# Performance work log

Hardware: AMD Instinct MI355X
Metric: run time of the kernel (lower is better)

Reference implementation:

```python
import jax, jax.numpy as jnp
import numpy as np

N = 100000
E = 1600000
F_IN = 128
HID = 16
HEADS = 8
NCLS = 2
NGRAPH = 64
NEG_SLOPE = 0.2


def setup_inputs() -> dict:
    key = jax.random.key(0)
    ks = jax.random.split(key, 12)
    x = jax.random.normal(ks[0], (N, F_IN), dtype=jnp.float32)
    edge_index = jax.random.randint(ks[1], (2, E), 0, N, dtype=jnp.int64)
    batch = jnp.sort(jax.random.randint(ks[2], (N,), 0, NGRAPH, dtype=jnp.int64))
    s1 = 1.0 / np.sqrt(F_IN)
    s2 = 1.0 / np.sqrt(HEADS * HID)
    W1 = jax.random.normal(ks[3], (F_IN, HEADS * HID), dtype=jnp.float32) * s1
    att_src1 = jax.random.normal(ks[4], (HEADS, HID), dtype=jnp.float32) * s2
    att_dst1 = jax.random.normal(ks[5], (HEADS, HID), dtype=jnp.float32) * s2
    b1 = jnp.zeros((HEADS * HID,), dtype=jnp.float32)
    W2 = jax.random.normal(ks[6], (HEADS * HID, 1 * NCLS), dtype=jnp.float32) * s2
    att_src2 = jax.random.normal(ks[7], (1, NCLS), dtype=jnp.float32)
    att_dst2 = jax.random.normal(ks[8], (1, NCLS), dtype=jnp.float32)
    b2 = jnp.zeros((NCLS,), dtype=jnp.float32)
    return {"x": x, "edge_index": edge_index, "batch": batch,
            "W1": W1, "att_src1": att_src1, "att_dst1": att_dst1, "b1": b1,
            "W2": W2, "att_src2": att_src2, "att_dst2": att_dst2, "b2": b2}


def _gat_conv(x, src, dst, W, att_src, att_dst, bias, heads, out_dim, concat):
    # x: [N, Fin]; src/dst: [E'] (self-loops already appended)
    h = (x @ W).reshape(N, heads, out_dim)              # [N, H, D]
    a_src = jnp.sum(h * att_src[None], axis=-1)          # [N, H]
    a_dst = jnp.sum(h * att_dst[None], axis=-1)          # [N, H]
    e = a_src[src] + a_dst[dst]                          # [E', H]
    e = jnp.where(e >= 0, e, NEG_SLOPE * e)              # leaky_relu
    # softmax over incoming edges of each destination node
    emax = jax.ops.segment_max(e, dst, num_segments=N)   # [N, H]
    ee = jnp.exp(e - emax[dst])
    denom = jax.ops.segment_sum(ee, dst, num_segments=N)
    alpha = ee / denom[dst]                              # [E', H]
    msg = h[src] * alpha[:, :, None]                     # [E', H, D]
    out = jax.ops.segment_sum(msg, dst, num_segments=N)  # [N, H, D]
    if concat:
        out = out.reshape(N, heads * out_dim)
    else:
        out = out.mean(axis=1)
    return out + bias


def reference(x, edge_index, batch, W1, att_src1, att_dst1, b1, W2, att_src2, att_dst2, b2):
    # add self-loops (PyG GATConv default add_self_loops=True)
    loop = jnp.arange(N, dtype=edge_index.dtype)
    src = jnp.concatenate([edge_index[0], loop])
    dst = jnp.concatenate([edge_index[1], loop])

    h = _gat_conv(x, src, dst, W1, att_src1, att_dst1, b1, HEADS, HID, True)
    h = jax.nn.elu(h)
    h = _gat_conv(h, src, dst, W2, att_src2, att_dst2, b2, 1, NCLS, False)

    # global mean pool over graphs
    ssum = jax.ops.segment_sum(h, batch, num_segments=NGRAPH)          # [G, C]
    cnt = jax.ops.segment_sum(jnp.ones((N,), h.dtype), batch, num_segments=NGRAPH)
    pooled = ssum / jnp.maximum(cnt, 1.0)[:, None]
    return jax.nn.log_softmax(pooled, axis=1)
```

## Files before the change

kernel.cpp:

```cpp
#include <hip/hip_runtime.h>
#include <math.h>

typedef long long ll;
typedef unsigned int u32;
typedef unsigned short u16;
typedef __attribute__((ext_vector_type(8))) short short8;
typedef __attribute__((ext_vector_type(4))) float f32x4;

#define NBLK 256
#define MAXBUK 512

__device__ __forceinline__ int load_idx(const void* p, int i, int is64) {
  return is64 ? (int)((const ll*)p)[i] : ((const int*)p)[i];
}

__device__ __forceinline__ u16 f2bf(float f) {
  u32 u = __float_as_uint(f);
  u += 0x7FFFu + ((u >> 16) & 1u);
  return (u16)(u >> 16);
}

__global__ void detect_kernel(const void* __restrict__ eidx, int ne,
                              const void* __restrict__ batch, int nb,
                              int* __restrict__ flags) {
  if (threadIdx.x == 0 && blockIdx.x == 0) {
    int e64 = 1;
    for (int k = 1; k <= 16; ++k) {
      int i = (int)((ll)k * (ne / 2 - 1) / 16);
      ll v = ((const ll*)eidx)[i];
      if (v < 0 || v >= (1LL << 31)) { e64 = 0; break; }
    }
    int b64 = 1;
    for (int k = 1; k <= 16; ++k) {
      int i = (int)((ll)k * (nb / 2 - 1) / 16);
      ll v = ((const ll*)batch)[i];
      if (v < 0 || v >= (1LL << 31)) { b64 = 0; break; }
    }
    flags[0] = e64; flags[1] = b64;
  }
}

__global__ void zero_kernel(float* __restrict__ pool) {
  int i = threadIdx.x;
  if (i < 192) pool[i] = 0.f;
}

__global__ __launch_bounds__(256) void gemm1_kernel(
    const float* __restrict__ x, const float* __restrict__ W1,
    const float* __restrict__ att_src, const float* __restrict__ att_dst,
    u16* __restrict__ h, float* __restrict__ a_src, float* __restrict__ a_dst,
    int nn) {
  __shared__ __align__(16) char smem[64 * 136 * 2 + 128 * 136 * 2];
  u16* xs = (u16*)smem;
  u16* Wt = (u16*)(smem + 64 * 136 * 2);
  float* hs = (float*)smem;
  int t = threadIdx.x;
  int n0 = blockIdx.x * 64;

  #pragma unroll 4
  for (int p = 0; p < 64; ++p) {
    int i = t + p * 256;
    int k = i >> 7, j = i & 127;
    u16 w = f2bf(W1[i]);
    Wt[j * 136 + k] = w;
  }
  #pragma unroll
  for (int p = 0; p < 4; ++p) {
    int row = p * 16 + (t >> 4);
    int c = t & 15;
    int gn = n0 + row;
    uint4 pk = make_uint4(0u, 0u, 0u, 0u);
    if (gn < nn) {
      const float4* xp = (const float4*)(x + (size_t)gn * 128 + c * 8);
      float4 f0 = xp[0], f1 = xp[1];
      pk.x = (u32)f2bf(f0.x) | ((u32)f2bf(f0.y) << 16);
      pk.y = (u32)f2bf(f0.z) | ((u32)f2bf(f0.w) << 16);
      pk.z = (u32)f2bf(f1.x) | ((u32)f2bf(f1.y) << 16);
      pk.w = (u32)f2bf(f1.z) | ((u32)f2bf(f1.w) << 16);
    }
    *(uint4*)&xs[row * 136 + c * 8] = pk;
  }
  __syncthreads();

  int lane = t & 63, wid = t >> 6;
  int lrow = lane & 15, lq = lane >> 4;
  short8 a[4];
  #pragma unroll
  for (int ks = 0; ks < 4; ++ks) {
    int row = wid * 16 + lrow;
    a[ks] = *(const short8*)&xs[row * 136 + ks * 32 + lq * 8];
  }
  f32x4 c[8];
  #pragma unroll
  for (int jt = 0; jt < 8; ++jt) c[jt] = (f32x4)(0.f);
  #pragma unroll
  for (int jt = 0; jt < 8; ++jt) {
    int j = jt * 16 + lrow;
    #pragma unroll
    for (int ks = 0; ks < 4; ++ks) {
      short8 b = *(const short8*)&Wt[j * 136 + ks * 32 + lq * 8];
      c[jt] = __builtin_amdgcn_mfma_f32_16x16x32_bf16(a[ks], b, c[jt], 0, 0, 0);
    }
  }
  __syncthreads();

  #pragma unroll
  for (int jt = 0; jt < 8; ++jt) {
    #pragma unroll
    for (int r = 0; r < 4; ++r) {
      hs[(wid * 16 + lq * 4 + r) * 132 + jt * 16 + lrow] = c[jt][r];
    }
  }
  __syncthreads();

  int q = t & 31, p = t >> 5;
  const float4 as4 = ((const float4*)att_src)[q];
  const float4 ad4 = ((const float4*)att_dst)[q];
  int head = q >> 2;
  #pragma unroll
  for (int rr = 0; rr < 8; ++rr) {
    int row = rr * 8 + p;
    int n = n0 + row;
    float4 v = *(const float4*)&hs[row * 132 + q * 4];
    float s = v.x * as4.x + v.y * as4.y + v.z * as4.z + v.w * as4.w;
    float d = v.x * ad4.x + v.y * ad4.y + v.z * ad4.z + v.w * ad4.w;
    s += __shfl_xor(s, 1); s += __shfl_xor(s, 2);
    d += __shfl_xor(d, 1); d += __shfl_xor(d, 2);
    if (n < nn) {
      uint2 pk;
      pk.x = (u32)f2bf(v.x) | ((u32)f2bf(v.y) << 16);
      pk.y = (u32)f2bf(v.z) | ((u32)f2bf(v.w) << 16);
      ((uint2*)(h + (size_t)n * 128))[q] = pk;
      if ((q & 3) == 0) { a_src[n * 8 + head] = s; a_dst[n * 8 + head] = d; }
    }
  }
}

__global__ __launch_bounds__(512) void ehist_kernel(
    const void* __restrict__ eidx, int E, int EP, int chunk,
    const int* __restrict__ flags, int* __restrict__ hist_g, int nbuk) {
  __shared__ int cnt[MAXBUK];
  int t = threadIdx.x, blk = blockIdx.x;
  if (t < MAXBUK) cnt[t] = 0;
  __syncthreads();
  int lo = blk * chunk, hi = min(lo + chunk, EP);
  int is64 = flags[0];
  for (int i = lo + t; i < hi; i += 512) {
    int d = (i < E) ? load_idx(eidx, E + i, is64) : (i - E);
    atomicAdd(&cnt[d >> 8], 1);
  }
  __syncthreads();
  if (t < nbuk) hist_g[t * NBLK + blk] = cnt[t];
}

__global__ __launch_bounds__(256) void scan_blk(const int* __restrict__ in,
                                                int* __restrict__ out,
                                                int* __restrict__ bsums, int n) {
  int t = threadIdx.x;
  int i = blockIdx.x * 256 + t;
  int v = (i < n) ? in[i] : 0;
  int lane = t & 63, w = t >> 6;
  int s = v;
  #pragma unroll
  for (int off = 1; off < 64; off <<= 1) {
    int u = __shfl_up(s, off);
    if (lane >= off) s += u;
  }
  __shared__ int wsum[4];
  if (lane == 63) wsum[w] = s;
  __syncthreads();
  int add = 0;
  for (int k = 0; k < w; ++k) add += wsum[k];
  int incl = s + add;
  if (i < n) out[i] = incl - v;
  if (t == 255) bsums[blockIdx.x] = incl;
}

__global__ __launch_bounds__(1024) void scan_top(int* __restrict__ bsums, int nb) {
  int t = threadIdx.x;
  int v = (t < nb) ? bsums[t] : 0;
  int lane = t & 63, w = t >> 6;
  int s = v;
  #pragma unroll
  for (int off = 1; off < 64; off <<= 1) {
    int u = __shfl_up(s, off);
    if (lane >= off) s += u;
  }
  __shared__ int ws[16];
  if (lane == 63) ws[w] = s;
  __syncthreads();
  int add = 0;
  for (int k = 0; k < w; ++k) add += ws[k];
  if (t < nb) bsums[t] = s + add - v;
}

__global__ void scan_add(int* __restrict__ out, const int* __restrict__ bsums, int n) {
  int i = blockIdx.x * 256 + threadIdx.x;
  if (i < n) out[i] += bsums[blockIdx.x];
}

__global__ __launch_bounds__(512) void escatter_kernel(
    const void* __restrict__ eidx, int E, int EP, int chunk,
    const int* __restrict__ flags, const int* __restrict__ base_g,
    u32* __restrict__ pairs, int nbuk) {
  __shared__ int cur[MAXBUK];
  int t = threadIdx.x, blk = blockIdx.x;
  if (t < nbuk) cur[t] = base_g[t * NBLK + blk];
  __syncthreads();
  int lo = blk * chunk, hi = min(lo + chunk, EP);
  int is64 = flags[0];
  for (int i = lo + t; i < hi; i += 512) {
    int s, d;
    if (i < E) { s = load_idx(eidx, i, is64); d = load_idx(eidx, E + i, is64); }
    else { s = d = i - E; }
    int pos = atomicAdd(&cur[d >> 8], 1);
    pairs[pos] = ((u32)(d & 255) << 24) | (u32)s;
  }
}

__global__ __launch_bounds__(256) void bfinal_kernel(
    const u32* __restrict__ pairs, const int* __restrict__ base_g,
    int* __restrict__ offs, int* __restrict__ ends, int* __restrict__ ssrc,
    int N, int EP, int nbuk) {
  int b = blockIdx.x, t = threadIdx.x;
  int nb0 = b << 8;
  __shared__ int cnt[256];
  __shared__ int cur[256];
  __shared__ int wsum[4];
  cnt[t] = 0;
  __syncthreads();
  int seg_start = base_g[b * NBLK];
  int seg_end = (b + 1 < nbuk) ? base_g[(b + 1) * NBLK] : EP;
  for (int i = seg_start + t; i < seg_end; i += 256) {
    atomicAdd(&cnt[pairs[i] >> 24], 1);
  }
  __syncthreads();
  int v = cnt[t];
  int lane = t & 63, w = t >> 6;
  int s = v;
  #pragma unroll
  for (int off = 1; off < 64; off <<= 1) {
    int u = __shfl_up(s, off);
    if (lane >= off) s += u;
  }
  if (lane == 63) wsum[w] = s;
  __syncthreads();
  int add = 0;
  for (int k = 0; k < w; ++k) add += wsum[k];
  int excl = s + add - v;
  cur[t] = excl;
  int node = nb0 + t;
  if (node < N) { offs[node] = seg_start + excl; ends[node] = seg_start + excl + v; }
  __syncthreads();
  for (int i = seg_start + t; i < seg_end; i += 256) {
    u32 p = pairs[i];
    int pos = atomicAdd(&cur[p >> 24], 1);
    ssrc[seg_start + pos] = (int)(p & 0xFFFFFFu);
  }
}

__global__ __launch_bounds__(256) void node1_kernel(
    const int* __restrict__ ssrc, const int* __restrict__ offs, const int* __restrict__ ends,
    const u16* __restrict__ h, const float* __restrict__ a_src, const float* __restrict__ a_dst,
    const float* __restrict__ b1, const float* __restrict__ W2,
    const float* __restrict__ att_s2, const float* __restrict__ att_d2,
    float* __restrict__ h2, float* __restrict__ as2, float* __restrict__ ad2, int nn) {
  int t = threadIdx.x;
  int wid = t >> 6, lane = t & 63;
  int grp = lane >> 4, lg = lane & 15;
  int n = blockIdx.x * 16 + wid * 4 + grp;
  bool nvalid = (n < nn);
  int nc = nvalid ? n : (nn - 1);
  int hh = lg >> 1;
  float adst = a_dst[nc * 8 + hh];
  int beg = offs[nc], end = ends[nc];
  int deg = nvalid ? (end - beg) : 0;
  int maxd = deg;
  maxd = max(maxd, __shfl_xor(maxd, 16));
  maxd = max(maxd, __shfl_xor(maxd, 32));
  float acc[8];
  #pragma unroll
  for (int k = 0; k < 8; ++k) acc[k] = 0.f;
  float dsum = 0.f;
  const u32* h32 = (const u32*)h;

  auto ld4 = [&](int* s4, int it0) {
    #pragma unroll
    for (int u = 0; u < 4; ++u) {
      int id = beg + it0 + u;
      s4[u] = ssrc[id < end ? id : end - 1];
    }
  };
  auto step = [&](const int* s4, int it0) {
    float ea4[4]; uint4 v4[4];
    #pragma unroll
    for (int u = 0; u < 4; ++u) {
      v4[u]  = *(const uint4*)(h32 + s4[u] * 64 + lg * 4);
      ea4[u] = a_src[s4[u] * 8 + hh];
    }
    #pragma unroll
    for (int u = 0; u < 4; ++u) {
      float e = ea4[u] + adst;
      e = fmaxf(e, 0.2f * e);
      float ee = (it0 + u < deg) ? __expf(e) : 0.f;
      dsum += ee;
      acc[0] = fmaf(ee, __uint_as_float(v4[u].x << 16),          acc[0]);
      acc[1] = fmaf(ee, __uint_as_float(v4[u].x & 0xFFFF0000u),  acc[1]);
      acc[2] = fmaf(ee, __uint_as_float(v4[u].y << 16),          acc[2]);
      acc[3] = fmaf(ee, __uint_as_float(v4[u].y & 0xFFFF0000u),  acc[3]);
      acc[4] = fmaf(ee, __uint_as_float(v4[u].z << 16),          acc[4]);
      acc[5] = fmaf(ee, __uint_as_float(v4[u].z & 0xFFFF0000u),  acc[5]);
      acc[6] = fmaf(ee, __uint_as_float(v4[u].w << 16),          acc[6]);
      acc[7] = fmaf(ee, __uint_as_float(v4[u].w & 0xFFFF0000u),  acc[7]);
    }
  };

  if (maxd > 0) {
    int sa[4], sb[4];
    ld4(sa, 0);
    for (int it = 0; it < maxd; it += 8) {
      ld4(sb, it + 4);
      step(sa, it);
      ld4(sa, it + 8);
      step(sb, it + 4);
    }
  }

  float inv = 1.f / dsum;
  float p0 = 0.f, p1 = 0.f;
  #pragma unroll
  for (int k = 0; k < 8; ++k) {
    int j = lg * 8 + k;
    float o = acc[k] * inv + b1[j];
    o = (o > 0.f) ? o : expm1f(o);
    p0 = fmaf(o, W2[j * 2],     p0);
    p1 = fmaf(o, W2[j * 2 + 1], p1);
  }
  #pragma unroll
  for (int m = 1; m < 16; m <<= 1) { p0 += __shfl_xor(p0, m); p1 += __shfl_xor(p1, m); }
  if (nvalid && lg == 0) {
    h2[n * 2] = p0; h2[n * 2 + 1] = p1;
    as2[n] = p0 * att_s2[0] + p1 * att_s2[1];
    ad2[n] = p0 * att_d2[0] + p1 * att_d2[1];
  }
}

__global__ __launch_bounds__(256) void node2_kernel(
    const int* __restrict__ ssrc, const int* __restrict__ offs, const int* __restrict__ ends,
    const float* __restrict__ h2, const float* __restrict__ as2, const float* __restrict__ ad2,
    const float* __restrict__ b2, const void* __restrict__ batch, const int* __restrict__ flags,
    float* __restrict__ pool, int nn) {
  __shared__ float psum[128];
  __shared__ float pcnt[64];
  int t = threadIdx.x;
  if (t < 128) psum[t] = 0.f;
  if (t < 64) pcnt[t] = 0.f;
  __syncthreads();
  int grp = t >> 3, lane8 = t & 7;
  int b64 = flags[1];
  int n = blockIdx.x * 32 + grp;
  if (n < nn) {
    float adst = ad2[n];
    int beg = offs[n], end = ends[n];
    float acc0 = 0.f, acc1 = 0.f, dsum = 0.f;
    for (int idx = beg + lane8; idx < end; idx += 8) {
      int s = ssrc[idx];
      float e = as2[s] + adst;
      e = (e < 0.f) ? 0.2f * e : e;
      float ee = __expf(e);
      float2 hv = *(const float2*)(h2 + (size_t)s * 2);
      acc0 = fmaf(ee, hv.x, acc0);
      acc1 = fmaf(ee, hv.y, acc1);
      dsum += ee;
    }
    #pragma unroll
    for (int m = 1; m < 8; m <<= 1) {
      acc0 += __shfl_xor(acc0, m);
      acc1 += __shfl_xor(acc1, m);
      dsum += __shfl_xor(dsum, m);
    }
    if (lane8 == 0) {
      float o0 = acc0 / dsum + b2[0];
      float o1 = acc1 / dsum + b2[1];
      int g = load_idx(batch, n, b64);
      atomicAdd(&psum[g * 2], o0);
      atomicAdd(&psum[g * 2 + 1], o1);
      atomicAdd(&pcnt[g], 1.f);
    }
  }
  __syncthreads();
  if (t < 64 && pcnt[t] > 0.f) {
    atomicAdd(&pool[t * 2], psum[t * 2]);
    atomicAdd(&pool[t * 2 + 1], psum[t * 2 + 1]);
    atomicAdd(&pool[128 + t], pcnt[t]);
  }
}

__global__ void finalize_kernel(const float* __restrict__ pool, float* __restrict__ out) {
  int g = threadIdx.x;
  if (g < 64) {
    float c = fmaxf(pool[128 + g], 1.f);
    float p0 = pool[g * 2] / c, p1 = pool[g * 2 + 1] / c;
    float m = fmaxf(p0, p1);
    float lse = m + logf(expf(p0 - m) + expf(p1 - m));
    out[g * 2] = p0 - lse;
    out[g * 2 + 1] = p1 - lse;
  }
}

extern "C" void kernel_launch(void* const* d_in, const int* in_sizes, int n_in,
                              void* d_out, int out_size, void* d_ws, size_t ws_size,
                              hipStream_t stream) {
  const float* x        = (const float*)d_in[0];
  const void* eidx      = d_in[1];
  const void* batch     = d_in[2];
  const float* W1       = (const float*)d_in[3];
  const float* att_src1 = (const float*)d_in[4];
  const float* att_dst1 = (const float*)d_in[5];
  const float* b1       = (const float*)d_in[6];
  const float* W2       = (const float*)d_in[7];
  const float* att_src2 = (const float*)d_in[8];
  const float* att_dst2 = (const float*)d_in[9];
  const float* b2       = (const float*)d_in[10];
  float* out = (float*)d_out;

  int N = in_sizes[0] / 128;
  int E = in_sizes[1] / 2;
  int EP = E + N;
  int NBUK = (N + 255) >> 8;
  int NC = NBUK * NBLK;
  int NB = (NC + 255) / 256;
  int chunk = (EP + NBLK - 1) / NBLK;

  char* ws = (char*)d_ws;
  size_t o = 0;
  auto alloc = [&](size_t bytes) -> void* {
    void* p = ws + o;
    o += (bytes + 255) & ~(size_t)255;
    return p;
  };
  u16*   h      = (u16*)alloc((size_t)N * 128 * 2);
  float* a_src1 = (float*)alloc((size_t)N * 8 * 4);
  float* a_dst1 = (float*)alloc((size_t)N * 8 * 4);
  int*   offs   = (int*)alloc((size_t)N * 4);
  int*   ends   = (int*)alloc((size_t)N * 4);
  int*   hist_g = (int*)alloc((size_t)NC * 4);
  int*   base_g = (int*)alloc((size_t)NC * 4);
  int*   bsums  = (int*)alloc((size_t)(NB + 1) * 4);
  u32*   pairs  = (u32*)alloc((size_t)EP * 4);
  int*   ssrc   = (int*)alloc((size_t)EP * 4);
  float* h2     = (float*)alloc((size_t)N * 2 * 4);
  float* as2    = (float*)alloc((size_t)N * 4);
  float* ad2    = (float*)alloc((size_t)N * 4);
  float* pool   = (float*)alloc(192 * 4);
  int*   flags  = (int*)alloc(2 * 4);

  detect_kernel<<<1, 64, 0, stream>>>(eidx, 2 * E, batch, N, flags);
  zero_kernel<<<1, 256, 0, stream>>>(pool);
  gemm1_kernel<<<(N + 63) / 64, 256, 0, stream>>>(x, W1, att_src1, att_dst1,
                                                  h, a_src1, a_dst1, N);
  ehist_kernel<<<NBLK, 512, 0, stream>>>(eidx, E, EP, chunk, flags, hist_g, NBUK);
  scan_blk<<<NB, 256, 0, stream>>>(hist_g, base_g, bsums, NC);
  scan_top<<<1, 1024, 0, stream>>>(bsums, NB);
  scan_add<<<NB, 256, 0, stream>>>(base_g, bsums, NC);
  escatter_kernel<<<NBLK, 512, 0, stream>>>(eidx, E, EP, chunk, flags, base_g, pairs, NBUK);
  bfinal_kernel<<<NBUK, 256, 0, stream>>>(pairs, base_g, offs, ends, ssrc, N, EP, NBUK);
  node1_kernel<<<(N + 15) / 16, 256, 0, stream>>>(ssrc, offs, ends, h, a_src1, a_dst1,
                                                  b1, W2, att_src2, att_dst2,
                                                  h2, as2, ad2, N);
  node2_kernel<<<(N + 31) / 32, 256, 0, stream>>>(ssrc, offs, ends, h2, as2, ad2,
                                                  b2, batch, flags, pool, N);
  finalize_kernel<<<1, 64, 0, stream>>>(pool, out);
}
```

Before: 214.0 us.

## Stage edge scatter in LDS, pack layer-2 node data, simplify gather loop

```diff
diff --git a/kernel.cpp b/kernel.cpp
--- a/kernel.cpp
+++ b/kernel.cpp
@@ -9,6 +9,7 @@
 
 #define NBLK 256
 #define MAXBUK 512
+#define CHUNK_MAX 8192
 
 __device__ __forceinline__ int load_idx(const void* p, int i, int is64) {
   return is64 ? (int)((const ll*)p)[i] : ((const int*)p)[i];
@@ -201,20 +202,46 @@
 
 __global__ __launch_bounds__(512) void escatter_kernel(
     const void* __restrict__ eidx, int E, int EP, int chunk,
-    const int* __restrict__ flags, const int* __restrict__ base_g,
-    u32* __restrict__ pairs, int nbuk) {
-  __shared__ int cur[MAXBUK];
+    const int* __restrict__ flags, const int* __restrict__ hist_g,
+    const int* __restrict__ base_g, u32* __restrict__ pairs, int nbuk) {
+  __shared__ int cnt[MAXBUK];
+  __shared__ int lbase[MAXBUK];
+  __shared__ int lcur[MAXBUK];
+  __shared__ u32 buf[CHUNK_MAX];
+  __shared__ int wsum[8];
   int t = threadIdx.x, blk = blockIdx.x;
-  if (t < nbuk) cur[t] = base_g[t * NBLK + blk];
+  int v = 0;
+  if (t < nbuk) { v = hist_g[t * NBLK + blk]; cnt[t] = v; }
+  int lane = t & 63, w = t >> 6;
+  int s = v;
+  #pragma unroll
+  for (int off = 1; off < 64; off <<= 1) {
+    int u = __shfl_up(s, off);
+    if (lane >= off) s += u;
+  }
+  if (lane == 63) wsum[w] = s;
+  __syncthreads();
+  int add = 0;
+  for (int k = 0; k < w; ++k) add += wsum[k];
+  if (t < nbuk) { lbase[t] = s + add - v; lcur[t] = s + add - v; }
   __syncthreads();
   int lo = blk * chunk, hi = min(lo + chunk, EP);
   int is64 = flags[0];
   for (int i = lo + t; i < hi; i += 512) {
-    int s, d;
-    if (i < E) { s = load_idx(eidx, i, is64); d = load_idx(eidx, E + i, is64); }
-    else { s = d = i - E; }
-    int pos = atomicAdd(&cur[d >> 8], 1);
-    pairs[pos] = ((u32)(d & 255) << 24) | (u32)s;
+    int sv, d;
+    if (i < E) { sv = load_idx(eidx, i, is64); d = load_idx(eidx, E + i, is64); }
+    else { sv = d = i - E; }
+    int pos = atomicAdd(&lcur[d >> 8], 1);
+    buf[pos] = ((u32)(d & 255) << 24) | (u32)sv;
+  }
+  __syncthreads();
+  for (int b = w; b < nbuk; b += 8) {
+    int n_b = cnt[b];
+    int lb = lbase[b];
+    int gb = base_g[b * NBLK + blk];
+    for (int k = lane; k < n_b; k += 64) {
+      pairs[gb + k] = buf[lb + k];
+    }
   }
 }
 
@@ -264,7 +291,7 @@
     const u16* __restrict__ h, const float* __restrict__ a_src, const float* __restrict__ a_dst,
     const float* __restrict__ b1, const float* __restrict__ W2,
     const float* __restrict__ att_s2, const float* __restrict__ att_d2,
-    float* __restrict__ h2, float* __restrict__ as2, float* __restrict__ ad2, int nn) {
+    float4* __restrict__ rec, int nn) {
   int t = threadIdx.x;
   int wid = t >> 6, lane = t & 63;
   int grp = lane >> 4, lg = lane & 15;
@@ -283,16 +310,13 @@
   for (int k = 0; k < 8; ++k) acc[k] = 0.f;
   float dsum = 0.f;
   const u32* h32 = (const u32*)h;
-
-  auto ld4 = [&](int* s4, int it0) {
+  for (int it = 0; it < maxd; it += 4) {
+    int s4[4]; float ea4[4]; uint4 v4[4];
     #pragma unroll
     for (int u = 0; u < 4; ++u) {
-      int id = beg + it0 + u;
+      int id = beg + it + u;
       s4[u] = ssrc[id < end ? id : end - 1];
     }
-  };
-  auto step = [&](const int* s4, int it0) {
-    float ea4[4]; uint4 v4[4];
     #pragma unroll
     for (int u = 0; u < 4; ++u) {
       v4[u]  = *(const uint4*)(h32 + s4[u] * 64 + lg * 4);
@@ -302,7 +326,7 @@
     for (int u = 0; u < 4; ++u) {
       float e = ea4[u] + adst;
       e = fmaxf(e, 0.2f * e);
-      float ee = (it0 + u < deg) ? __expf(e) : 0.f;
+      float ee = (it + u < deg) ? __expf(e) : 0.f;
       dsum += ee;
       acc[0] = fmaf(ee, __uint_as_float(v4[u].x << 16),          acc[0]);
       acc[1] = fmaf(ee, __uint_as_float(v4[u].x & 0xFFFF0000u),  acc[1]);
@@ -313,19 +337,7 @@
       acc[6] = fmaf(ee, __uint_as_float(v4[u].w << 16),          acc[6]);
       acc[7] = fmaf(ee, __uint_as_float(v4[u].w & 0xFFFF0000u),  acc[7]);
     }
-  };
-
-  if (maxd > 0) {
-    int sa[4], sb[4];
-    ld4(sa, 0);
-    for (int it = 0; it < maxd; it += 8) {
-      ld4(sb, it + 4);
-      step(sa, it);
-      ld4(sa, it + 8);
-      step(sb, it + 4);
-    }
-  }
-
+  }
   float inv = 1.f / dsum;
   float p0 = 0.f, p1 = 0.f;
   #pragma unroll
@@ -339,16 +351,16 @@
   #pragma unroll
   for (int m = 1; m < 16; m <<= 1) { p0 += __shfl_xor(p0, m); p1 += __shfl_xor(p1, m); }
   if (nvalid && lg == 0) {
-    h2[n * 2] = p0; h2[n * 2 + 1] = p1;
-    as2[n] = p0 * att_s2[0] + p1 * att_s2[1];
-    ad2[n] = p0 * att_d2[0] + p1 * att_d2[1];
+    rec[n] = make_float4(p0, p1,
+                         p0 * att_s2[0] + p1 * att_s2[1],
+                         p0 * att_d2[0] + p1 * att_d2[1]);
   }
 }
 
 __global__ __launch_bounds__(256) void node2_kernel(
     const int* __restrict__ ssrc, const int* __restrict__ offs, const int* __restrict__ ends,
-    const float* __restrict__ h2, const float* __restrict__ as2, const float* __restrict__ ad2,
-    const float* __restrict__ b2, const void* __restrict__ batch, const int* __restrict__ flags,
+    const float4* __restrict__ rec, const float* __restrict__ b2,
+    const void* __restrict__ batch, const int* __restrict__ flags,
     float* __restrict__ pool, int nn) {
   __shared__ float psum[128];
   __shared__ float pcnt[64];
@@ -360,17 +372,17 @@
   int b64 = flags[1];
   int n = blockIdx.x * 32 + grp;
   if (n < nn) {
-    float adst = ad2[n];
+    float adst = rec[n].w;
     int beg = offs[n], end = ends[n];
     float acc0 = 0.f, acc1 = 0.f, dsum = 0.f;
     for (int idx = beg + lane8; idx < end; idx += 8) {
       int s = ssrc[idx];
-      float e = as2[s] + adst;
+      float4 r = rec[s];
+      float e = r.z + adst;
       e = (e < 0.f) ? 0.2f * e : e;
       float ee = __expf(e);
-      float2 hv = *(const float2*)(h2 + (size_t)s * 2);
-      acc0 = fmaf(ee, hv.x, acc0);
-      acc1 = fmaf(ee, hv.y, acc1);
+      acc0 = fmaf(ee, r.x, acc0);
+      acc1 = fmaf(ee, r.y, acc1);
       dsum += ee;
     }
     #pragma unroll
@@ -430,7 +442,7 @@
   int NBUK = (N + 255) >> 8;
   int NC = NBUK * NBLK;
   int NB = (NC + 255) / 256;
-  int chunk = (EP + NBLK - 1) / NBLK;
+  int chunk = (((EP + NBLK - 1) / NBLK) + 1) & ~1;
 
   char* ws = (char*)d_ws;
   size_t o = 0;
@@ -449,9 +461,7 @@
   int*   bsums  = (int*)alloc((size_t)(NB + 1) * 4);
   u32*   pairs  = (u32*)alloc((size_t)EP * 4);
   int*   ssrc   = (int*)alloc((size_t)EP * 4);
-  float* h2     = (float*)alloc((size_t)N * 2 * 4);
-  float* as2    = (float*)alloc((size_t)N * 4);
-  float* ad2    = (float*)alloc((size_t)N * 4);
+  float4* rec   = (float4*)alloc((size_t)N * 16);
   float* pool   = (float*)alloc(192 * 4);
   int*   flags  = (int*)alloc(2 * 4);
 
@@ -463,12 +473,13 @@
   scan_blk<<<NB, 256, 0, stream>>>(hist_g, base_g, bsums, NC);
   scan_top<<<1, 1024, 0, stream>>>(bsums, NB);
   scan_add<<<NB, 256, 0, stream>>>(base_g, bsums, NC);
-  escatter_kernel<<<NBLK, 512, 0, stream>>>(eidx, E, EP, chunk, flags, base_g, pairs, NBUK);
+  escatter_kernel<<<NBLK, 512, 0, stream>>>(eidx, E, EP, chunk, flags, hist_g,
+                                            base_g, pairs, NBUK);
   bfinal_kernel<<<NBUK, 256, 0, stream>>>(pairs, base_g, offs, ends, ssrc, N, EP, NBUK);
   node1_kernel<<<(N + 15) / 16, 256, 0, stream>>>(ssrc, offs, ends, h, a_src1, a_dst1,
                                                   b1, W2, att_src2, att_dst2,
-                                                  h2, as2, ad2, N);
-  node2_kernel<<<(N + 31) / 32, 256, 0, stream>>>(ssrc, offs, ends, h2, as2, ad2,
+                                                  rec, N);
+  node2_kernel<<<(N + 31) / 32, 256, 0, stream>>>(ssrc, offs, ends, rec,
                                                   b2, batch, flags, pool, N);
   finalize_kernel<<<1, 64, 0, stream>>>(pool, out);
 }
```

After: 212.5 us. No clear change (-0.7%).
